# Kernel tuning notes

Hardware: AMD Instinct MI355X
Metric: run time of the kernel (lower is better)

The kernel has to match this reference:

```python
import jax, jax.numpy as jnp
import numpy as np
import math

B, C, N = 8, 512, 2048

def setup_inputs() -> dict:
    key = jax.random.key(0)
    ks = jax.random.split(key, 7)
    s = 0.02
    return {
        "x": jax.random.normal(ks[0], (B, C, N), dtype=jnp.float32),
        "Wq": jax.random.normal(ks[1], (C // 2, C), dtype=jnp.float32) * s,
        "bq": jax.random.normal(ks[2], (C // 2,), dtype=jnp.float32) * s,
        "Wk": jax.random.normal(ks[3], (C // 2, C), dtype=jnp.float32) * s,
        "bk": jax.random.normal(ks[4], (C // 2,), dtype=jnp.float32) * s,
        "Wv": jax.random.normal(ks[5], (C, C), dtype=jnp.float32) * s,
        "bv": jax.random.normal(ks[6], (C,), dtype=jnp.float32) * s,
    }

def reference(x, Wq, bq, Wk, bk, Wv, bv):
    # pointwise conv1d == channel matmul: (O,C) x (B,C,N) -> (B,O,N)
    Q = jnp.einsum('oc,bcn->bon', Wq, x) + bq[None, :, None]  # (B, C/2, N)
    K = jnp.einsum('oc,bcn->bon', Wk, x) + bk[None, :, None]  # (B, C/2, N)
    V = jnp.einsum('oc,bcn->bon', Wv, x) + bv[None, :, None]  # (B, C, N)
    scale = 1.0 / math.sqrt(K.shape[1])
    A = jnp.einsum('bcn,bcm->bnm', Q, K) * scale              # (B, N, N)
    A = jax.nn.softmax(A, axis=-1)
    out = jnp.einsum('bcm,bnm->bcn', V, A)                    # V @ A^T
    return x + out
```

## Files before the change

### kernel.cpp

```cpp
#include <hip/hip_runtime.h>

#define B_ 8
#define C_ 512
#define N_ 2048
#define O_ 256

typedef unsigned short u16;
typedef unsigned char u8;
typedef unsigned int uint;
typedef float f32x4 __attribute__((ext_vector_type(4)));
typedef int i32x8 __attribute__((ext_vector_type(8)));

#define AS1 __attribute__((address_space(1)))
#define AS3 __attribute__((address_space(3)))

__device__ __forceinline__ u16 f2bf(float f) {
  union { float f; unsigned u; } v; v.f = f;
  return (u16)((v.u + 0x7fffu + ((v.u >> 16) & 1u)) >> 16);
}
__device__ __forceinline__ float bf2f(u16 h) {
  union { uint u; float f; } v; v.u = ((uint)h) << 16; return v.f;
}
__device__ __forceinline__ uint pk4_e4m3(float a, float b, float c, float d) {
  int r = __builtin_amdgcn_cvt_pk_fp8_f32(a, b, 0, false);
  r = __builtin_amdgcn_cvt_pk_fp8_f32(c, d, r, true);
  return (uint)r;
}

union MxFrag { i32x8 v; uint4 q[2]; };

__device__ __forceinline__ f32x4 mxmfma(const MxFrag& a, const MxFrag& b,
                                        f32x4 c) {
  return __builtin_amdgcn_mfma_scale_f32_16x16x128_f8f6f4(
      a.v, b.v, c,
      0, 0,
      0, 0x7f7f7f7f,
      0, 0x7f7f7f7f);
}

template<int R>
__device__ __forceinline__ MxFrag readFrag(const u8 (&S)[R][128], int row,
                                           int quad, int swz) {
  MxFrag f;
  const u8* rp = &S[row][0];
  const int g0 = (quad * 2) ^ swz, g1 = (quad * 2 + 1) ^ swz;
  f.q[0] = *(const uint4*)(rp + g0 * 16);
  f.q[1] = *(const uint4*)(rp + g1 * 16);
  return f;
}

template<int AR>
__device__ __forceinline__ void mx_stage_tile(
    const u8* __restrict__ Ag, int lda,
    const u8* __restrict__ Bg, int ldb, int k0,
    u8 (&As)[AR][128], u8 (&Bs)[128][128], int w, int r8, int gsrc)
{
#pragma unroll
  for (int s = 0; s < AR / 32; s++) {
    int row = (w * (AR / 32) + s) * 8;
    __builtin_amdgcn_global_load_lds(
        (const AS1 uint*)(Ag + (size_t)(row + r8) * lda + k0 + gsrc * 16),
        (AS3 uint*)(&As[row][0]), 16, 0, 0);
  }
#pragma unroll
  for (int s = 0; s < 4; s++) {
    int row = (w * 4 + s) * 8;
    __builtin_amdgcn_global_load_lds(
        (const AS1 uint*)(Bg + (size_t)(row + r8) * ldb + k0 + gsrc * 16),
        (AS3 uint*)(&Bs[row][0]), 16, 0, 0);
  }
}

template<int MI, int AR>
__device__ __forceinline__ void mx_compute_tile(
    const u8 (&As)[AR][128], const u8 (&Bs)[128][128],
    f32x4 (&acc)[MI][4], int wm, int wn, int lrow, int quad)
{
  const int swz = lrow & 7;
  MxFrag af[MI], bfr[4];
#pragma unroll
  for (int i = 0; i < MI; i++)
    af[i] = readFrag(As, wm + i * 16 + lrow, quad, swz);
#pragma unroll
  for (int j = 0; j < 4; j++)
    bfr[j] = readFrag(Bs, wn + j * 16 + lrow, quad, swz);
  asm volatile("s_waitcnt lgkmcnt(0)" ::: "memory");
#pragma unroll
  for (int i = 0; i < MI; i++)
#pragma unroll
    for (int j = 0; j < 4; j++)
      acc[i][j] = mxmfma(af[i], bfr[j], acc[i][j]);
}

template<int NT, int AR, int MI>
__device__ __forceinline__ void mx_mainloop_db(
    const u8* __restrict__ Ag, int lda,
    const u8* __restrict__ Bg, int ldb,
    u8 (&As)[2][AR][128], u8 (&Bs)[2][128][128],
    f32x4 (&acc)[MI][4], int wm, int wn)
{
  const int t = threadIdx.x;
  const int lane = t & 63;
  const int w = t >> 6;
  const int lrow = lane & 15, quad = lane >> 4;
  const int r8 = lane >> 3;
  const int gsrc = (lane & 7) ^ r8;
  constexpr int LPT = AR / 32 + 4;

  mx_stage_tile<AR>(Ag, lda, Bg, ldb, 0, As[0], Bs[0], w, r8, gsrc);
  if (NT > 1)
    mx_stage_tile<AR>(Ag, lda, Bg, ldb, 128, As[1], Bs[1], w, r8, gsrc);

#pragma unroll
  for (int tt = 0; tt < NT; ++tt) {
    if (tt + 1 < NT)
      asm volatile("s_waitcnt vmcnt(%0)" :: "n"(LPT) : "memory");
    else
      asm volatile("s_waitcnt vmcnt(0)" ::: "memory");
    __builtin_amdgcn_s_barrier();
    mx_compute_tile<MI, AR>(As[tt & 1], Bs[tt & 1], acc, wm, wn, lrow, quad);
    __builtin_amdgcn_s_barrier();
    if (tt + 2 < NT)
      mx_stage_tile<AR>(Ag, lda, Bg, ldb, (tt + 2) * 128,
                        As[tt & 1], Bs[tt & 1], w, r8, gsrc);
  }
}

__global__ __launch_bounds__(256) void prep_kernel(
    const float* __restrict__ x,
    const float* __restrict__ Wq, const float* __restrict__ Wk,
    const float* __restrict__ Wv,
    u8* __restrict__ xT8, u8* __restrict__ Wq8, u8* __restrict__ Wk8,
    u8* __restrict__ Wv8)
{
  __shared__ u16 tile[64][72];
  const int bid = blockIdx.x;
  const int t = threadIdx.x;
  if (bid < 2048) {
    int b = bid >> 8;
    int n0 = (bid & 31) * 64;
    int c0 = ((bid >> 5) & 7) * 64;
    const float* src = x + (size_t)b * C_ * N_ + (size_t)c0 * N_ + n0;
    int r = t >> 4;
    int f4 = (t & 15) * 4;
#pragma unroll
    for (int i = 0; i < 4; i++) {
      int c = r + 16 * i;
      float4 v = *(const float4*)(src + (size_t)c * N_ + f4);
      tile[f4 + 0][c] = f2bf(v.x);
      tile[f4 + 1][c] = f2bf(v.y);
      tile[f4 + 2][c] = f2bf(v.z);
      tile[f4 + 3][c] = f2bf(v.w);
    }
    __syncthreads();
    u8* dst = xT8 + (size_t)b * N_ * C_ + (size_t)n0 * C_ + c0;
    int n = t >> 2;
    int cc = (t & 3) * 16;
    uint4 d;
    d.x = pk4_e4m3(bf2f(tile[n][cc + 0]), bf2f(tile[n][cc + 1]),
                   bf2f(tile[n][cc + 2]), bf2f(tile[n][cc + 3]));
    d.y = pk4_e4m3(bf2f(tile[n][cc + 4]), bf2f(tile[n][cc + 5]),
                   bf2f(tile[n][cc + 6]), bf2f(tile[n][cc + 7]));
    d.z = pk4_e4m3(bf2f(tile[n][cc + 8]), bf2f(tile[n][cc + 9]),
                   bf2f(tile[n][cc + 10]), bf2f(tile[n][cc + 11]));
    d.w = pk4_e4m3(bf2f(tile[n][cc + 12]), bf2f(tile[n][cc + 13]),
                   bf2f(tile[n][cc + 14]), bf2f(tile[n][cc + 15]));
    *(uint4*)(dst + (size_t)n * C_ + cc) = d;
  } else {
    int gid = (bid - 2048) * 256 + t;
    const float* src; u8* dst; int o;
    if (gid < 32768)      { src = Wq; dst = Wq8; o = gid; }
    else if (gid < 65536) { src = Wk; dst = Wk8; o = gid - 32768; }
    else                  { src = Wv; dst = Wv8; o = gid - 65536; }
    float4 v = *(const float4*)(src + (size_t)o * 4);
    *(uint*)(dst + (size_t)o * 4) = pk4_e4m3(v.x, v.y, v.z, v.w);
  }
}

__global__ __launch_bounds__(256) void proj_all_kernel(
    const u8* __restrict__ xT8,
    const u8* __restrict__ Wq8, const float* __restrict__ bq,
    const u8* __restrict__ Wk8, const float* __restrict__ bk,
    const u8* __restrict__ Wv8, const float* __restrict__ bv,
    u8* __restrict__ Qt8, u8* __restrict__ Kt8, u8* __restrict__ V8)
{
  __shared__ __align__(16) u8 As[2][128][128], Bs[2][128][128];
  const int n0 = blockIdx.x * 128;
  const int b = blockIdx.y;
  const int sub = blockIdx.z;
  const u8* xTb = xT8 + (size_t)b * N_ * C_ + (size_t)n0 * C_;

  const f32x4 zero = {0.f, 0.f, 0.f, 0.f};
  f32x4 acc[4][4];
#pragma unroll
  for (int i = 0; i < 4; i++)
#pragma unroll
    for (int j = 0; j < 4; j++) acc[i][j] = zero;

  const int lane = threadIdx.x & 63;
  const int w = threadIdx.x >> 6;
  const int wm = (w >> 1) * 64, wn = (w & 1) * 64;
  const int quad = lane >> 4, lcol = lane & 15;

  if (sub < 4) {
    const int isK = sub >> 1;
    const int o0 = (sub & 1) * 128;
    const u8* Wg = (isK ? Wk8 : Wq8) + (size_t)o0 * C_;
    const float* bias = isK ? bk : bq;
    u8* outp = (isK ? Kt8 : Qt8) + (size_t)b * N_ * O_;

    mx_mainloop_db<4, 128, 4>(Wg, C_, xTb, C_, As, Bs, acc, wm, wn);

#pragma unroll
    for (int i = 0; i < 4; i++) {
      int obase = o0 + wm + i * 16 + quad * 4;
      float4 bb = *(const float4*)(bias + obase);
#pragma unroll
      for (int j = 0; j < 4; j++) {
        int n = n0 + wn + j * 16 + lcol;
        uint d = pk4_e4m3(acc[i][j][0] + bb.x, acc[i][j][1] + bb.y,
                          acc[i][j][2] + bb.z, acc[i][j][3] + bb.w);
        *(uint*)(outp + (size_t)n * O_ + obase) = d;
      }
    }
  } else {
    const int c0 = (sub - 4) * 128;
    const u8* Wg = Wv8 + (size_t)c0 * C_;
    u8* outp = V8 + (size_t)b * C_ * N_;

    mx_mainloop_db<4, 128, 4>(xTb, C_, Wg, C_, As, Bs, acc, wm, wn);

#pragma unroll
    for (int j = 0; j < 4; j++) {
      int c = c0 + wn + j * 16 + lcol;
      float bb = bv[c];
#pragma unroll
      for (int i = 0; i < 4; i++) {
        int nbase = n0 + wm + i * 16 + quad * 4;
        uint d = pk4_e4m3(acc[i][j][0] + bb, acc[i][j][1] + bb,
                          acc[i][j][2] + bb, acc[i][j][3] + bb);
        *(uint*)(outp + (size_t)c * N_ + nbase) = d;
      }
    }
  }
}

__global__ __launch_bounds__(512, 2) void attn_fused_kernel(
    const u8* __restrict__ Qt8, const u8* __restrict__ Kt8,
    const u8* __restrict__ V8, const float* __restrict__ x,
    float* __restrict__ out)
{
  __shared__ __align__(16) u8 Qs[2][128][128];
  __shared__ __align__(16) u8 Ks[2][128][128];
  __shared__ __align__(16) u8 Vs[256][128];
  __shared__ __align__(16) u8 Ps[128][128];
  __shared__ float rsum2[4][128];

  const int L = blockIdx.x + (int)(blockIdx.y * gridDim.x) +
                (int)(blockIdx.z * gridDim.x * gridDim.y);
  const int b = L & 7;
  const int c0 = ((L >> 3) & 1) * 256;
  const int n0 = (L >> 4) * 128;

  const u8* Qb = Qt8 + (size_t)b * N_ * O_ + (size_t)n0 * O_;
  const u8* Kb = Kt8 + (size_t)b * N_ * O_;
  const u8* Vg = V8 + (size_t)b * C_ * N_ + (size_t)c0 * N_;

  const int t = threadIdx.x;
  const int lane = t & 63;
  const int w = t >> 6;
  const int lrow = lane & 15, quad = lane >> 4;
  const int swz = lrow & 7;
  const int r8 = lane >> 3;
  const int gsrc = (lane & 7) ^ r8;
  const int wm_s = (w & 3) * 32;
  const int wn   = (w >> 2) * 64;
  const int wm_o = (w & 3) * 64;

  auto stageQ = [&]() {
#pragma unroll
    for (int s = 0; s < 4; s++) {
      int idx = w * 4 + s;
      int ch = idx >> 4, row = (idx & 15) * 8;
      __builtin_amdgcn_global_load_lds(
          (const AS1 uint*)(Qb + (size_t)(row + r8) * O_ + ch * 128 + gsrc * 16),
          (AS3 uint*)(&Qs[ch][row][0]), 16, 0, 0);
    }
  };
  auto stageK = [&](int m0) {
#pragma unroll
    for (int s = 0; s < 4; s++) {
      int idx = w * 4 + s;
      int ch = idx >> 4, row = (idx & 15) * 8;
      __builtin_amdgcn_global_load_lds(
          (const AS1 uint*)(Kb + (size_t)(m0 + row + r8) * O_ + ch * 128 + gsrc * 16),
          (AS3 uint*)(&Ks[ch][row][0]), 16, 0, 0);
    }
  };
  auto stageV = [&](int m0) {
#pragma unroll
    for (int s = 0; s < 4; s++) {
      int idx = w * 4 + s;
      int row = idx * 8;
      __builtin_amdgcn_global_load_lds(
          (const AS1 uint*)(Vg + (size_t)(row + r8) * N_ + m0 + gsrc * 16),
          (AS3 uint*)(&Vs[row][0]), 16, 0, 0);
    }
  };

  stageQ();
  stageK(0);
  stageV(0);
  asm volatile("s_waitcnt vmcnt(8)" ::: "memory");
  __builtin_amdgcn_s_barrier();

  MxFrag qf[2][4];
#pragma unroll
  for (int ch = 0; ch < 2; ch++)
#pragma unroll
    for (int j = 0; j < 4; j++)
      qf[ch][j] = readFrag(Qs[ch], wn + j * 16 + lrow, quad, swz);

  const f32x4 zero = {0.f, 0.f, 0.f, 0.f};
  f32x4 acco[4][4];
#pragma unroll
  for (int i = 0; i < 4; i++)
#pragma unroll
    for (int j = 0; j < 4; j++) acco[i][j] = zero;
  float partial[4] = {0.f, 0.f, 0.f, 0.f};

#pragma unroll 1
  for (int mt = 0; mt < 16; ++mt) {
    asm volatile("s_waitcnt vmcnt(4)" ::: "memory");
    __builtin_amdgcn_s_barrier();

    f32x4 accs[2][4];
#pragma unroll
    for (int i = 0; i < 2; i++)
#pragma unroll
      for (int j = 0; j < 4; j++) accs[i][j] = zero;
#pragma unroll
    for (int ch = 0; ch < 2; ch++) {
      MxFrag a0 = readFrag(Ks[ch], wm_s + lrow, quad, swz);
      MxFrag a1 = readFrag(Ks[ch], wm_s + 16 + lrow, quad, swz);
#pragma unroll
      for (int j = 0; j < 4; j++) {
        accs[0][j] = mxmfma(a0, qf[ch][j], accs[0][j]);
        accs[1][j] = mxmfma(a1, qf[ch][j], accs[1][j]);
      }
    }
#pragma unroll
    for (int i = 0; i < 2; i++) {
      const int mb = wm_s + i * 16 + quad * 4;
      const int gw = mb >> 4;
#pragma unroll
      for (int j = 0; j < 4; j++) {
        const int n = wn + j * 16 + lrow;
        float p0 = __expf(accs[i][j][0] * 0.0625f);
        float p1 = __expf(accs[i][j][1] * 0.0625f);
        float p2 = __expf(accs[i][j][2] * 0.0625f);
        float p3 = __expf(accs[i][j][3] * 0.0625f);
        partial[j] += (p0 + p1) + (p2 + p3);
        *(uint*)(&Ps[n][((gw ^ (n & 7)) << 4) | (quad * 4)]) =
            pk4_e4m3(p0, p1, p2, p3);
      }
    }
    asm volatile("s_waitcnt lgkmcnt(0) vmcnt(0)" ::: "memory");
    __builtin_amdgcn_s_barrier();
    if (mt + 1 < 16) stageK((mt + 1) * 128);

    MxFrag vf[4], pf[4];
#pragma unroll
    for (int i = 0; i < 4; i++)
      vf[i] = readFrag(Vs, wm_o + i * 16 + lrow, quad, swz);
#pragma unroll
    for (int j = 0; j < 4; j++)
      pf[j] = readFrag(Ps, wn + j * 16 + lrow, quad, swz);
#pragma unroll
    for (int i = 0; i < 4; i++)
#pragma unroll
      for (int j = 0; j < 4; j++)
        acco[i][j] = mxmfma(vf[i], pf[j], acco[i][j]);
    asm volatile("s_waitcnt lgkmcnt(0)" ::: "memory");
    __builtin_amdgcn_s_barrier();
    if (mt + 1 < 16) stageV((mt + 1) * 128);
  }

#pragma unroll
  for (int msk = 16; msk < 64; msk <<= 1)
#pragma unroll
    for (int j = 0; j < 4; j++) partial[j] += __shfl_xor(partial[j], msk);
  if (quad == 0)
#pragma unroll
    for (int j = 0; j < 4; j++)
      rsum2[w & 3][wn + j * 16 + lrow] = partial[j];
  __syncthreads();

  float invl[4];
#pragma unroll
  for (int j = 0; j < 4; j++) {
    const int n = wn + j * 16 + lrow;
    invl[j] = 1.f / (rsum2[0][n] + rsum2[1][n] + rsum2[2][n] + rsum2[3][n]);
  }
  const float* xb = x + (size_t)b * C_ * N_;
  float* ob = out + (size_t)b * C_ * N_;
#pragma unroll
  for (int i = 0; i < 4; i++)
#pragma unroll
    for (int rr = 0; rr < 4; rr++) {
      const int cg = c0 + wm_o + i * 16 + quad * 4 + rr;
#pragma unroll
      for (int j = 0; j < 4; j++) {
        const int ng = n0 + wn + j * 16 + lrow;
        const size_t idx = (size_t)cg * N_ + ng;
        ob[idx] = xb[idx] + acco[i][j][rr] * invl[j];
      }
    }
}

extern "C" void kernel_launch(void* const* d_in, const int* in_sizes, int n_in,
                              void* d_out, int out_size, void* d_ws, size_t ws_size,
                              hipStream_t stream)
{
  (void)in_sizes; (void)n_in; (void)out_size; (void)ws_size;
  const float* x  = (const float*)d_in[0];
  const float* Wq = (const float*)d_in[1];
  const float* bq = (const float*)d_in[2];
  const float* Wk = (const float*)d_in[3];
  const float* bk = (const float*)d_in[4];
  const float* Wv = (const float*)d_in[5];
  const float* bv = (const float*)d_in[6];
  float* out = (float*)d_out;

  char* ws = (char*)d_ws;
  size_t off = 0;
  auto carve = [&](size_t bytes) -> char* {
    char* p = ws + off;
    off += (bytes + 255) & ~(size_t)255;
    return p;
  };
  u8*  xT8  = (u8*) carve((size_t)B_ * N_ * C_);
  u8*  Wq8  = (u8*) carve((size_t)O_ * C_);
  u8*  Wk8  = (u8*) carve((size_t)O_ * C_);
  u8*  Wv8  = (u8*) carve((size_t)C_ * C_);
  u8*  Qt8  = (u8*) carve((size_t)B_ * N_ * O_);
  u8*  Kt8  = (u8*) carve((size_t)B_ * N_ * O_);
  u8*  Vb   = (u8*) carve((size_t)B_ * C_ * N_);

  prep_kernel<<<dim3(2560), 256, 0, stream>>>(
      x, Wq, Wk, Wv, xT8, Wq8, Wk8, Wv8);
  proj_all_kernel<<<dim3(N_ / 128, B_, 8), 256, 0, stream>>>(
      xT8, Wq8, bq, Wk8, bk, Wv8, bv, Qt8, Kt8, Vb);
  attn_fused_kernel<<<dim3(N_ / 128, 2, B_), 512, 0, stream>>>(
      Qt8, Kt8, Vb, x, out);
}
```

Baseline: 175.9 us.

## Halve attention query tile to 64 and cut LDS to raise occupancy

Shrinks the per-block query tile from 128 to 64 columns, doubling the grid, and drops the separate Q and rowsum LDS buffers: Q is staged through the K buffer before the loop, the P tile is halved, and row sums reuse the P buffer. Launch bounds go from 2 to 4 blocks per CU so more blocks can be resident to hide latency. The cost is that K and V tiles are now loaded from global memory twice as often per query, and each block does half the MFMA work per barrier.

```diff
diff --git a/kernel.cpp b/kernel.cpp
--- a/kernel.cpp
+++ b/kernel.cpp
@@ -245,22 +245,20 @@
   }
 }
 
-__global__ __launch_bounds__(512, 2) void attn_fused_kernel(
+__global__ __launch_bounds__(512, 4) void attn_fused_kernel(
     const u8* __restrict__ Qt8, const u8* __restrict__ Kt8,
     const u8* __restrict__ V8, const float* __restrict__ x,
     float* __restrict__ out)
 {
-  __shared__ __align__(16) u8 Qs[2][128][128];
   __shared__ __align__(16) u8 Ks[2][128][128];
   __shared__ __align__(16) u8 Vs[256][128];
-  __shared__ __align__(16) u8 Ps[128][128];
-  __shared__ float rsum2[4][128];
+  __shared__ __align__(16) u8 Ps[64][128];
 
   const int L = blockIdx.x + (int)(blockIdx.y * gridDim.x) +
                 (int)(blockIdx.z * gridDim.x * gridDim.y);
   const int b = L & 7;
   const int c0 = ((L >> 3) & 1) * 256;
-  const int n0 = (L >> 4) * 128;
+  const int n0 = (L >> 4) * 64;
 
   const u8* Qb = Qt8 + (size_t)b * N_ * O_ + (size_t)n0 * O_;
   const u8* Kb = Kt8 + (size_t)b * N_ * O_;
@@ -274,19 +272,9 @@
   const int r8 = lane >> 3;
   const int gsrc = (lane & 7) ^ r8;
   const int wm_s = (w & 3) * 32;
-  const int wn   = (w >> 2) * 64;
+  const int wns  = (w >> 2) * 32;
   const int wm_o = (w & 3) * 64;
 
-  auto stageQ = [&]() {
-#pragma unroll
-    for (int s = 0; s < 4; s++) {
-      int idx = w * 4 + s;
-      int ch = idx >> 4, row = (idx & 15) * 8;
-      __builtin_amdgcn_global_load_lds(
-          (const AS1 uint*)(Qb + (size_t)(row + r8) * O_ + ch * 128 + gsrc * 16),
-          (AS3 uint*)(&Qs[ch][row][0]), 16, 0, 0);
-    }
-  };
   auto stageK = [&](int m0) {
 #pragma unroll
     for (int s = 0; s < 4; s++) {
@@ -308,43 +296,53 @@
     }
   };
 
-  stageQ();
+#pragma unroll
+  for (int s = 0; s < 2; s++) {
+    int idx = w * 2 + s;
+    int ch = idx >> 3, row = (idx & 7) * 8;
+    __builtin_amdgcn_global_load_lds(
+        (const AS1 uint*)(Qb + (size_t)(row + r8) * O_ + ch * 128 + gsrc * 16),
+        (AS3 uint*)(&Ks[ch][row][0]), 16, 0, 0);
+  }
+  asm volatile("s_waitcnt vmcnt(0)" ::: "memory");
+  __builtin_amdgcn_s_barrier();
+
+  MxFrag qf[2][2];
+#pragma unroll
+  for (int ch = 0; ch < 2; ch++)
+#pragma unroll
+    for (int j = 0; j < 2; j++)
+      qf[ch][j] = readFrag(Ks[ch], wns + j * 16 + lrow, quad, swz);
+  asm volatile("s_waitcnt lgkmcnt(0)" ::: "memory");
+  __builtin_amdgcn_s_barrier();
+
   stageK(0);
   stageV(0);
-  asm volatile("s_waitcnt vmcnt(8)" ::: "memory");
-  __builtin_amdgcn_s_barrier();
-
-  MxFrag qf[2][4];
-#pragma unroll
-  for (int ch = 0; ch < 2; ch++)
-#pragma unroll
-    for (int j = 0; j < 4; j++)
-      qf[ch][j] = readFrag(Qs[ch], wn + j * 16 + lrow, quad, swz);
 
   const f32x4 zero = {0.f, 0.f, 0.f, 0.f};
-  f32x4 acco[4][4];
+  f32x4 acco[4][2];
 #pragma unroll
   for (int i = 0; i < 4; i++)
 #pragma unroll
-    for (int j = 0; j < 4; j++) acco[i][j] = zero;
-  float partial[4] = {0.f, 0.f, 0.f, 0.f};
+    for (int j = 0; j < 2; j++) acco[i][j] = zero;
+  float partial[2] = {0.f, 0.f};
 
 #pragma unroll 1
   for (int mt = 0; mt < 16; ++mt) {
     asm volatile("s_waitcnt vmcnt(4)" ::: "memory");
     __builtin_amdgcn_s_barrier();
 
-    f32x4 accs[2][4];
+    f32x4 accs[2][2];
 #pragma unroll
     for (int i = 0; i < 2; i++)
 #pragma unroll
-      for (int j = 0; j < 4; j++) accs[i][j] = zero;
+      for (int j = 0; j < 2; j++) accs[i][j] = zero;
 #pragma unroll
     for (int ch = 0; ch < 2; ch++) {
       MxFrag a0 = readFrag(Ks[ch], wm_s + lrow, quad, swz);
       MxFrag a1 = readFrag(Ks[ch], wm_s + 16 + lrow, quad, swz);
 #pragma unroll
-      for (int j = 0; j < 4; j++) {
+      for (int j = 0; j < 2; j++) {
         accs[0][j] = mxmfma(a0, qf[ch][j], accs[0][j]);
         accs[1][j] = mxmfma(a1, qf[ch][j], accs[1][j]);
       }
@@ -354,8 +352,8 @@
       const int mb = wm_s + i * 16 + quad * 4;
       const int gw = mb >> 4;
 #pragma unroll
-      for (int j = 0; j < 4; j++) {
-        const int n = wn + j * 16 + lrow;
+      for (int j = 0; j < 2; j++) {
+        const int n = wns + j * 16 + lrow;
         float p0 = __expf(accs[i][j][0] * 0.0625f);
         float p1 = __expf(accs[i][j][1] * 0.0625f);
         float p2 = __expf(accs[i][j][2] * 0.0625f);
@@ -369,38 +367,41 @@
     __builtin_amdgcn_s_barrier();
     if (mt + 1 < 16) stageK((mt + 1) * 128);
 
-    MxFrag vf[4], pf[4];
-#pragma unroll
-    for (int i = 0; i < 4; i++)
-      vf[i] = readFrag(Vs, wm_o + i * 16 + lrow, quad, swz);
-#pragma unroll
-    for (int j = 0; j < 4; j++)
-      pf[j] = readFrag(Ps, wn + j * 16 + lrow, quad, swz);
-#pragma unroll
-    for (int i = 0; i < 4; i++)
-#pragma unroll
-      for (int j = 0; j < 4; j++)
-        acco[i][j] = mxmfma(vf[i], pf[j], acco[i][j]);
+    {
+      MxFrag vf[4];
+#pragma unroll
+      for (int i = 0; i < 4; i++)
+        vf[i] = readFrag(Vs, wm_o + i * 16 + lrow, quad, swz);
+#pragma unroll
+      for (int j = 0; j < 2; j++) {
+        MxFrag pf = readFrag(Ps, wns + j * 16 + lrow, quad, swz);
+#pragma unroll
+        for (int i = 0; i < 4; i++)
+          acco[i][j] = mxmfma(vf[i], pf, acco[i][j]);
+      }
+    }
     asm volatile("s_waitcnt lgkmcnt(0)" ::: "memory");
     __builtin_amdgcn_s_barrier();
     if (mt + 1 < 16) stageV((mt + 1) * 128);
   }
 
+  float* rsumF = (float*)&Ps[0][0];
 #pragma unroll
   for (int msk = 16; msk < 64; msk <<= 1)
 #pragma unroll
-    for (int j = 0; j < 4; j++) partial[j] += __shfl_xor(partial[j], msk);
+    for (int j = 0; j < 2; j++) partial[j] += __shfl_xor(partial[j], msk);
   if (quad == 0)
 #pragma unroll
-    for (int j = 0; j < 4; j++)
-      rsum2[w & 3][wn + j * 16 + lrow] = partial[j];
+    for (int j = 0; j < 2; j++)
+      rsumF[(w & 3) * 64 + wns + j * 16 + lrow] = partial[j];
   __syncthreads();
 
-  float invl[4];
-#pragma unroll
-  for (int j = 0; j < 4; j++) {
-    const int n = wn + j * 16 + lrow;
-    invl[j] = 1.f / (rsum2[0][n] + rsum2[1][n] + rsum2[2][n] + rsum2[3][n]);
+  float invl[2];
+#pragma unroll
+  for (int j = 0; j < 2; j++) {
+    const int nn = wns + j * 16 + lrow;
+    invl[j] = 1.f / (rsumF[nn] + rsumF[64 + nn] + rsumF[128 + nn] +
+                     rsumF[192 + nn]);
   }
   const float* xb = x + (size_t)b * C_ * N_;
   float* ob = out + (size_t)b * C_ * N_;
@@ -410,8 +411,8 @@
     for (int rr = 0; rr < 4; rr++) {
       const int cg = c0 + wm_o + i * 16 + quad * 4 + rr;
 #pragma unroll
-      for (int j = 0; j < 4; j++) {
-        const int ng = n0 + wn + j * 16 + lrow;
+      for (int j = 0; j < 2; j++) {
+        const int ng = n0 + wns + j * 16 + lrow;
         const size_t idx = (size_t)cg * N_ + ng;
         ob[idx] = xb[idx] + acco[i][j][rr] * invl[j];
       }
@@ -451,6 +452,6 @@
       x, Wq, Wk, Wv, xT8, Wq8, Wk8, Wv8);
   proj_all_kernel<<<dim3(N_ / 128, B_, 8), 256, 0, stream>>>(
       xT8, Wq8, bq, Wk8, bk, Wv8, bv, Qt8, Kt8, Vb);
-  attn_fused_kernel<<<dim3(N_ / 128, 2, B_), 512, 0, stream>>>(
+  attn_fused_kernel<<<dim3(N_ / 64, 2, B_), 512, 0, stream>>>(
       Qt8, Kt8, Vb, x, out);
 }
```

Result: slower. 212.5 us (+20.8%).
